# Kernel optimization log

Measured on AMD Instinct MI355X. Metric: run time of the kernel, lower is better.

Reference implementation:

```python
import jax, jax.numpy as jnp
import numpy as np

N, C, OUT, S, NS = 8192, 256, 256, 8, 16  # points, in_planes, out_planes, share_planes, nsample
MID = OUT  # mid_planes = out_planes // 1
H = OUT // S  # linear_w bottleneck width
EPS = 1e-5


def _bn(x, g, b, m, v):
    # inference-mode BatchNorm1d over last (channel) dim
    return (x - m) * jax.lax.rsqrt(v + EPS) * g + b


def _knn_idx(p, k):
    # squared euclidean distances, (N,N); indices of k nearest (self included)
    sq = jnp.sum(p * p, axis=1)
    d = sq[:, None] + sq[None, :] - 2.0 * (p @ p.T)
    return jax.lax.top_k(-jax.lax.stop_gradient(d), k)[1]  # (N, k) int32


def setup_inputs() -> dict:
    key = jax.random.key(0)
    ks = jax.random.split(key, 24)
    g = lambda i, shape, s=0.05: jax.random.normal(ks[i], shape, jnp.float32) * s
    u = lambda i, shape: jax.random.uniform(ks[i], shape, dtype=jnp.float32)
    return {
        'p': u(0, (N, 3)),
        'x': g(1, (N, C), 1.0),
        'w_q': g(2, (C, MID)), 'b_q': jnp.zeros((MID,), jnp.float32),
        'w_k': g(3, (C, MID)), 'b_k': jnp.zeros((MID,), jnp.float32),
        'w_v': g(4, (C, OUT)), 'b_v': jnp.zeros((OUT,), jnp.float32),
        'p_w1': g(5, (3, 3), 0.5), 'p_b1': jnp.zeros((3,), jnp.float32),
        'p_bn_g': u(6, (3,)) + 0.5, 'p_bn_b': g(7, (3,), 0.1),
        'p_bn_m': g(8, (3,), 0.1), 'p_bn_v': u(9, (3,)) + 0.5,
        'p_w2': g(10, (3, OUT), 0.5), 'p_b2': jnp.zeros((OUT,), jnp.float32),
        'w_bn1_g': u(11, (MID,)) + 0.5, 'w_bn1_b': g(12, (MID,), 0.1),
        'w_bn1_m': g(13, (MID,), 0.1), 'w_bn1_v': u(14, (MID,)) + 0.5,
        'w_l1_w': g(15, (MID, H)), 'w_l1_b': jnp.zeros((H,), jnp.float32),
        'w_bn2_g': u(16, (H,)) + 0.5, 'w_bn2_b': g(17, (H,), 0.1),
        'w_bn2_m': g(18, (H,), 0.1), 'w_bn2_v': u(19, (H,)) + 0.5,
        'w_l2_w': g(20, (H, H)), 'w_l2_b': jnp.zeros((H,), jnp.float32),
    }


def reference(p, x, w_q, b_q, w_k, b_k, w_v, b_v,
              p_w1, p_b1, p_bn_g, p_bn_b, p_bn_m, p_bn_v, p_w2, p_b2,
              w_bn1_g, w_bn1_b, w_bn1_m, w_bn1_v, w_l1_w, w_l1_b,
              w_bn2_g, w_bn2_b, w_bn2_m, w_bn2_v, w_l2_w, w_l2_b):
    # PointTransformerLayer forward (single point cloud, o = [N])
    xq = x @ w_q + b_q            # (N, MID)
    xk = x @ w_k + b_k            # (N, MID)
    xv = x @ w_v + b_v            # (N, OUT)

    idx = _knn_idx(p, NS)         # (N, NS) KNN neighbor indices
    pr_xyz = p[idx] - p[:, None, :]   # (N, NS, 3) relative coords (with_xyz=True)
    xk_g = xk[idx]                # (N, NS, MID) gathered keys
    xv_g = xv[idx]                # (N, NS, OUT) gathered values

    # linear_p: Linear(3,3) -> BN -> ReLU -> Linear(3, OUT)
    pr = jax.nn.relu(_bn(pr_xyz @ p_w1 + p_b1, p_bn_g, p_bn_b, p_bn_m, p_bn_v))
    pr = pr @ p_w2 + p_b2         # (N, NS, OUT)

    # einops reduce 'n ns (i j)->n ns j' with j=MID is identity since MID==OUT
    r_qk = xk_g - xq[:, None, :] + pr   # (N, NS, MID)

    # linear_w: BN -> ReLU -> Linear(MID,H) -> BN -> ReLU -> Linear(H,H)
    w = jax.nn.relu(_bn(r_qk, w_bn1_g, w_bn1_b, w_bn1_m, w_bn1_v)) @ w_l1_w + w_l1_b
    w = jax.nn.relu(_bn(w, w_bn2_g, w_bn2_b, w_bn2_m, w_bn2_v)) @ w_l2_w + w_l2_b
    w = jax.nn.softmax(w, axis=1)       # softmax over neighbors (dim=1)

    v = (xv_g + pr).reshape(N, NS, S, H)      # 'n ns (s i) -> n ns s i'
    out = jnp.einsum('ntsi,nti->nsi', v, w)   # weighted aggregation over neighbors
    return out.reshape(N, OUT)
```

## Files before the change

### kernel.cpp

```cpp
#include <hip/hip_runtime.h>
#include <hip/hip_bf16.h>
#include <math.h>

#define N_PTS 8192
#define C_IN  256
#define OUT_C 256
#define NSAMP 16
#define H_W   32
#define EPSBN 1e-5f
#define GDIM  8
#define NCELL (GDIM * GDIM * GDIM)
#define CAPC  768
#define CAP_H 40

typedef short bf16x8 __attribute__((ext_vector_type(8)));
typedef float f32x4  __attribute__((ext_vector_type(4)));

__device__ __forceinline__ float dist2(const float4 a, const float4 b) {
  float dot = a.x * b.x + a.y * b.y + a.z * b.z;
  return a.w + b.w - 2.0f * dot;
}

__device__ __forceinline__ unsigned long long make_key(float d, int j) {
  unsigned int di = __float_as_uint(d);
  unsigned int ord = ((int)di >= 0) ? (di ^ 0x80000000u) : ~di;
  return ((unsigned long long)ord << 32) | (unsigned int)j;
}

__device__ __forceinline__ void chain_insert(unsigned long long (&ak)[16], unsigned long long key) {
  if (key < ak[0]) {
    #pragma unroll
    for (int s = 0; s < 15; ++s) {
      unsigned long long mn = ak[s] < key ? ak[s] : key;
      unsigned long long nx = ak[s + 1];
      ak[s] = nx > mn ? nx : mn;
    }
    ak[15] = ak[15] < key ? ak[15] : key;
  }
}

__device__ __forceinline__ void merge16f(float (&A)[16], int m) {
  float B[16], t[16];
  #pragma unroll
  for (int s = 0; s < 16; ++s) B[s] = __shfl_xor(A[s], m, 64);
  #pragma unroll
  for (int s = 0; s < 16; ++s) t[s] = fminf(A[s], B[15 - s]);
  #pragma unroll
  for (int k = 8; k >= 1; k >>= 1) {
    #pragma unroll
    for (int s = 0; s < 16; ++s) {
      if (!(s & k)) {
        float lo = fminf(t[s], t[s | k]);
        float hi = fmaxf(t[s], t[s | k]);
        t[s] = lo; t[s | k] = hi;
      }
    }
  }
  #pragma unroll
  for (int s = 0; s < 16; ++s) A[s] = t[s];
}

__global__ __launch_bounds__(256) void prep_kernel(
    const float* __restrict__ p,
    const float* __restrict__ wq, const float* __restrict__ wk, const float* __restrict__ wv,
    const float* __restrict__ bq, const float* __restrict__ bk, const float* __restrict__ bv,
    const float* __restrict__ l1w, const float* __restrict__ l2w,
    float4* __restrict__ p4, __hip_bfloat16* __restrict__ Bp, float* __restrict__ biasp,
    __hip_bfloat16* __restrict__ l1wp, __hip_bfloat16* __restrict__ l2wp,
    int* __restrict__ hist, int* __restrict__ pt_cell) {
  int tid = blockIdx.x * blockDim.x + threadIdx.x;
  if (tid < 48 * 32 * 16 * 8) {
    int kj = tid & 7, n = (tid >> 3) & 15, kb = (tid >> 7) & 31, nt = tid >> 12;
    int k = kb * 8 + kj, col = nt * 16 + n;
    float v;
    if (col < 256)      v = wq[k * 256 + col];
    else if (col < 512) v = wk[k * 256 + (col - 256)];
    else                v = wv[k * 256 + (col - 512)];
    Bp[tid] = __float2bfloat16(v);
  }
  if (tid < 768) {
    biasp[tid] = tid < 256 ? bq[tid] : (tid < 512 ? bk[tid - 256] : bv[tid - 512]);
  }
  if (tid < 8192) {
    int kj = tid & 7, n = (tid >> 3) & 15, kb = (tid >> 7) & 31, nt = (tid >> 12) & 1;
    int k = kb * 8 + kj, col = nt * 16 + n;
    l1wp[tid] = __float2bfloat16(l1w[k * 32 + col]);
  }
  if (tid < 1024) {
    int kj = tid & 7, n = (tid >> 3) & 15, kb = (tid >> 7) & 3, nt = (tid >> 9) & 1;
    int k = kb * 8 + kj, col = nt * 16 + n;
    l2wp[tid] = __float2bfloat16(l2w[k * 32 + col]);
  }
  if (tid < N_PTS) {
    float px = p[tid * 3 + 0], py = p[tid * 3 + 1], pz = p[tid * 3 + 2];
    float sq = px * px;
    sq += py * py;
    sq += pz * pz;
    p4[tid] = make_float4(px, py, pz, sq);
    int cx = min(GDIM - 1, max(0, (int)(px * GDIM)));
    int cy = min(GDIM - 1, max(0, (int)(py * GDIM)));
    int cz = min(GDIM - 1, max(0, (int)(pz * GDIM)));
    int cell = (cz * GDIM + cy) * GDIM + cx;
    pt_cell[tid] = cell;
    atomicAdd(&hist[cell], 1);
  }
}

__global__ __launch_bounds__(512) void scan512(const int* __restrict__ hist, int* __restrict__ cell_start) {
  __shared__ int buf[NCELL];
  int t = threadIdx.x;
  buf[t] = hist[t];
  __syncthreads();
  for (int off = 1; off < NCELL; off <<= 1) {
    int add = (t >= off) ? buf[t - off] : 0;
    __syncthreads();
    buf[t] += add;
    __syncthreads();
  }
  cell_start[t + 1] = buf[t];
  if (t == 0) cell_start[0] = 0;
}

__global__ __launch_bounds__(256) void scatter_kernel(
    const float4* __restrict__ p4, const int* __restrict__ pt_cell,
    const int* __restrict__ cell_start, int* __restrict__ cursor,
    float4* __restrict__ sp4, int* __restrict__ sidx, int* __restrict__ rank) {
  int tid = blockIdx.x * blockDim.x + threadIdx.x;
  if (tid < N_PTS) {
    int c = pt_cell[tid];
    int pos = cell_start[c] + atomicAdd(&cursor[c], 1);
    sp4[pos] = p4[tid];
    sidx[pos] = tid;
    rank[tid] = pos;
  }
}

__global__ __launch_bounds__(256) void xbf_kernel(
    const float* __restrict__ x, const int* __restrict__ sidx,
    __hip_bfloat16* __restrict__ x_bf) {
  const int b = blockIdx.x;
  const int c = threadIdx.x;
  x_bf[(size_t)b * C_IN + c] = __float2bfloat16(x[(size_t)sidx[b] * C_IN + c]);
}

__global__ __launch_bounds__(256) void knn_grid(
    const float4* __restrict__ sp4, const int* __restrict__ sidx,
    const int* __restrict__ cell_start, int* __restrict__ nbr) {
  __shared__ float4 cpos[CAPC];
  __shared__ int    cidx[CAPC];
  __shared__ unsigned long long hk_s[8][CAP_H];
  __shared__ unsigned long long okey_s[8][16];
  __shared__ int cnt_s[8];
  __shared__ int cell_s0_s[27];
  __shared__ int len_s[27];
  __shared__ int pref_s[28];
  __shared__ int nc_s, total_s;

  const int cell = blockIdx.x >> 1;
  const int sub  = blockIdx.x & 1;
  const int tid = threadIdx.x;
  const int hcx = cell & 7, hcy = (cell >> 3) & 7, hcz = cell >> 6;
  const int cs = cell_start[cell], ce = cell_start[cell + 1];

  const int ax0 = max(hcx - 1, 0), ax1 = min(hcx + 1, GDIM - 1);
  const int ay0 = max(hcy - 1, 0), ay1 = min(hcy + 1, GDIM - 1);
  const int az0 = max(hcz - 1, 0), az1 = min(hcz + 1, GDIM - 1);
  const int nx = ax1 - ax0 + 1, ny = ay1 - ay0 + 1, nz = az1 - az0 + 1;
  const int nbc = nx * ny * nz;

  if (tid < nbc) {
    int cx = ax0 + tid % nx;
    int cy = ay0 + (tid / nx) % ny;
    int cz = az0 + tid / (nx * ny);
    int cc = (cz * GDIM + cy) * GDIM + cx;
    int s0 = cell_start[cc];
    cell_s0_s[tid] = s0;
    len_s[tid] = cell_start[cc + 1] - s0;
  }
  __syncthreads();
  if (tid == 0) {
    int off = 0;
    for (int m = 0; m < nbc; ++m) { pref_s[m] = off; off += len_s[m]; }
    pref_s[nbc] = off;
    nc_s = nbc;
    total_s = off;
  }
  __syncthreads();
  const int nc = nc_s, total = total_s;

  for (int idx = tid; idx < total && idx < CAPC; idx += 256) {
    int c = 0;
    while (c + 1 < nc && pref_s[c + 1] <= idx) ++c;
    int g = cell_s0_s[c] + (idx - pref_s[c]);
    cpos[idx] = sp4[g];
    cidx[idx] = sidx[g];
  }
  __syncthreads();

  const int ptl = tid >> 5, slice = tid & 31;

  for (int p0 = cs + 8 * sub; p0 < ce; p0 += 16) {
    const int np = min(8, ce - p0);
    const bool pok = ptl < np;
    const int ld = pok ? (p0 + ptl) : cs;
    const float4 pi = sp4[ld];
    const int orig = sidx[ld];

    if (tid < 8) cnt_s[tid] = 0;
    if (tid < 128) okey_s[tid >> 4][tid & 15] = ~0ULL;
    __syncthreads();

    float a[16];
    #pragma unroll
    for (int s = 0; s < 16; ++s) a[s] = 3.0e38f;
    for (int idx = slice; idx < total; idx += 32) {
      float4 q;
      if (idx < CAPC) q = cpos[idx];
      else {
        int c = 0;
        while (c + 1 < nc && pref_s[c + 1] <= idx) ++c;
        q = sp4[cell_s0_s[c] + (idx - pref_s[c])];
      }
      float d = dist2(pi, q);
      if (d < a[0]) {
        #pragma unroll
        for (int s = 0; s < 15; ++s) a[s] = fmaxf(a[s + 1], fminf(a[s], d));
        a[15] = fminf(a[15], d);
      }
    }
    float asc[16];
    #pragma unroll
    for (int s = 0; s < 16; ++s) asc[s] = a[15 - s];
    merge16f(asc, 1);
    merge16f(asc, 2);
    merge16f(asc, 4);
    merge16f(asc, 8);
    merge16f(asc, 16);
    const float d16 = asc[15];

    if (pok) {
      for (int idx = slice; idx < total; idx += 32) {
        float4 q;
        int qi;
        if (idx < CAPC) { q = cpos[idx]; qi = cidx[idx]; }
        else {
          int c = 0;
          while (c + 1 < nc && pref_s[c + 1] <= idx) ++c;
          int g = cell_s0_s[c] + (idx - pref_s[c]);
          q = sp4[g]; qi = sidx[g];
        }
        float d = dist2(pi, q);
        if (d <= d16) {
          int pos = atomicAdd(&cnt_s[ptl], 1);
          if (pos < CAP_H) hk_s[ptl][pos] = make_key(d, qi);
        }
      }
    }
    __syncthreads();

    const int cntr = cnt_s[ptl];
    const bool overflow = cntr > CAP_H;
    const int cnt = overflow ? 0 : cntr;

    if (pok) {
      for (int i = slice; i < cnt; i += 32) {
        unsigned long long key = hk_s[ptl][i];
        int rk = 0;
        for (int j = 0; j < cnt; ++j) rk += (hk_s[ptl][j] < key) ? 1 : 0;
        if (rk < 16) okey_s[ptl][rk] = key;
      }
    }
    __syncthreads();

    if (slice == 0 && pok) {
      unsigned long long akm[16];
      if (!overflow) {
        #pragma unroll
        for (int s = 0; s < 16; ++s) akm[s] = okey_s[ptl][15 - s];
      } else {
        #pragma unroll
        for (int s = 0; s < 16; ++s) akm[s] = ~0ULL;
        for (int idx = 0; idx < total; ++idx) {
          float4 q; int qi;
          if (idx < CAPC) { q = cpos[idx]; qi = cidx[idx]; }
          else {
            int c = 0;
            while (c + 1 < nc && pref_s[c + 1] <= idx) ++c;
            int g = cell_s0_s[c] + (idx - pref_s[c]);
            q = sp4[g]; qi = sidx[g];
          }
          chain_insert(akm, make_key(dist2(pi, q), qi));
        }
      }
      float r;
      if (akm[0] == ~0ULL) {
        r = 1e9f;
      } else {
        unsigned int ord = (unsigned int)(akm[0] >> 32);
        unsigned int di = (ord & 0x80000000u) ? (ord ^ 0x80000000u) : ~ord;
        float dd = __uint_as_float(di);
        r = sqrtf(fmaxf(dd, 0.f)) * 1.001f + 1e-4f;
      }
      int lx = (int)fminf(fmaxf(floorf((pi.x - r) * GDIM), 0.f), (float)(GDIM - 1));
      int ux = (int)fminf(fmaxf(floorf((pi.x + r) * GDIM), 0.f), (float)(GDIM - 1));
      int ly = (int)fminf(fmaxf(floorf((pi.y - r) * GDIM), 0.f), (float)(GDIM - 1));
      int uy = (int)fminf(fmaxf(floorf((pi.y + r) * GDIM), 0.f), (float)(GDIM - 1));
      int lz = (int)fminf(fmaxf(floorf((pi.z - r) * GDIM), 0.f), (float)(GDIM - 1));
      int uz = (int)fminf(fmaxf(floorf((pi.z + r) * GDIM), 0.f), (float)(GDIM - 1));
      if (lx < ax0 || ux > ax1 || ly < ay0 || uy > ay1 || lz < az0 || uz > az1) {
        for (int cz = lz; cz <= uz; ++cz)
          for (int cy = ly; cy <= uy; ++cy)
            for (int cx = lx; cx <= ux; ++cx) {
              if (cx >= ax0 && cx <= ax1 && cy >= ay0 && cy <= ay1 && cz >= az0 && cz <= az1)
                continue;
              int cc = (cz * GDIM + cy) * GDIM + cx;
              int s0 = cell_start[cc], e0 = cell_start[cc + 1];
              for (int k = s0; k < e0; ++k) {
                float4 q = sp4[k];
                chain_insert(akm, make_key(dist2(pi, q), sidx[k]));
              }
            }
      }
      #pragma unroll
      for (int s = 0; s < 16; ++s) nbr[orig * NSAMP + s] = (int)(akm[s] & 0xFFFFFFFFu);
    }
    __syncthreads();
  }
}

__global__ __launch_bounds__(256) void gemm_qkv_mfma(
    const __hip_bfloat16* __restrict__ x_bf, const __hip_bfloat16* __restrict__ Bp,
    const float* __restrict__ biasp, __hip_bfloat16* __restrict__ xqkv) {
  const int w = threadIdx.x >> 6;
  const int lane = threadIdx.x & 63;
  const int gw = blockIdx.x * 4 + w;
  const int m0 = (gw & 127) * 64;
  const int nt4 = (gw >> 7) * 4;
  const int n = lane & 15, q = lane >> 4;

  f32x4 acc[4][4];
  #pragma unroll
  for (int mi = 0; mi < 4; ++mi)
    #pragma unroll
    for (int ni = 0; ni < 4; ++ni) acc[mi][ni] = (f32x4){0.f, 0.f, 0.f, 0.f};

  for (int k0 = 0; k0 < 256; k0 += 32) {
    bf16x8 af[4], bfr[4];
    #pragma unroll
    for (int mi = 0; mi < 4; ++mi)
      af[mi] = *(const bf16x8*)&x_bf[(size_t)(m0 + mi * 16 + n) * 256 + k0 + q * 8];
    #pragma unroll
    for (int ni = 0; ni < 4; ++ni)
      bfr[ni] = *(const bf16x8*)&Bp[(size_t)(nt4 + ni) * 4096 + (k0 >> 3) * 128 + q * 128 + n * 8];
    #pragma unroll
    for (int mi = 0; mi < 4; ++mi)
      #pragma unroll
      for (int ni = 0; ni < 4; ++ni)
        acc[mi][ni] = __builtin_amdgcn_mfma_f32_16x16x32_bf16(af[mi], bfr[ni], acc[mi][ni], 0, 0, 0);
  }
  #pragma unroll
  for (int ni = 0; ni < 4; ++ni) {
    int col = (nt4 + ni) * 16 + n;
    float b = biasp[col];
    #pragma unroll
    for (int mi = 0; mi < 4; ++mi)
      #pragma unroll
      for (int r = 0; r < 4; ++r)
        xqkv[(size_t)(m0 + mi * 16 + q * 4 + r) * 768 + col] = __float2bfloat16(acc[mi][ni][r] + b);
  }
}

__global__ __launch_bounds__(256) void fused_pt(
    const float4* __restrict__ sp4, const int* __restrict__ sidx, const int* __restrict__ rank,
    const __hip_bfloat16* __restrict__ xqkv, const int* __restrict__ nbr,
    const float* __restrict__ pw1, const float* __restrict__ pb1,
    const float* __restrict__ pbng, const float* __restrict__ pbnb,
    const float* __restrict__ pbnm, const float* __restrict__ pbnv,
    const float* __restrict__ pw2, const float* __restrict__ pb2,
    const float* __restrict__ bn1g, const float* __restrict__ bn1b,
    const float* __restrict__ bn1m, const float* __restrict__ bn1v,
    const __hip_bfloat16* __restrict__ l1wp, const float* __restrict__ l1b,
    const float* __restrict__ bn2g, const float* __restrict__ bn2b,
    const float* __restrict__ bn2m, const float* __restrict__ bn2v,
    const __hip_bfloat16* __restrict__ l2wp, const float* __restrict__ l2b,
    float* __restrict__ out) {
  __shared__ __align__(16) __hip_bfloat16 a_s[NSAMP][264];
  __shared__ __align__(16) __hip_bfloat16 h1_s[NSAMP][40];
  __shared__ float w_s[NSAMP][33];
  __shared__ float q3_s[NSAMP][4];
  __shared__ int jn[NSAMP];

  const int b = blockIdx.x;
  const int i = sidx[b];
  const int tid = threadIdx.x;

  if (tid < NSAMP) {
    int j = nbr[i * NSAMP + tid];
    int k = rank[j];
    jn[tid] = k;
    float4 pj = sp4[k];
    float4 pc = sp4[b];
    float rx = pj.x - pc.x;
    float ry = pj.y - pc.y;
    float rz = pj.z - pc.z;
    #pragma unroll
    for (int c3 = 0; c3 < 3; ++c3) {
      float t = rx * pw1[0 * 3 + c3] + ry * pw1[1 * 3 + c3] + rz * pw1[2 * 3 + c3] + pb1[c3];
      t = (t - pbnm[c3]) * rsqrtf(pbnv[c3] + EPSBN) * pbng[c3] + pbnb[c3];
      q3_s[tid][c3] = fmaxf(t, 0.f);
    }
  }
  __syncthreads();

  const int c = tid;
  const float xq_c = __bfloat162float(xqkv[(size_t)b * 768 + c]);
  const float s1 = bn1g[c] * rsqrtf(bn1v[c] + EPSBN);
  const float o1 = bn1b[c] - bn1m[c] * s1;
  const float w2c0 = pw2[c], w2c1 = pw2[256 + c], w2c2 = pw2[512 + c];
  const float pb2c = pb2[c];
  #pragma unroll
  for (int t = 0; t < NSAMP; ++t) {
    int k = jn[t];
    float prv = q3_s[t][0] * w2c0 + q3_s[t][1] * w2c1 + q3_s[t][2] * w2c2 + pb2c;
    float xkv = __bfloat162float(xqkv[(size_t)k * 768 + 256 + c]);
    float r = xkv - xq_c + prv;
    a_s[t][c] = __float2bfloat16(fmaxf(r * s1 + o1, 0.f));
  }
  __syncthreads();

  const int wv_ = tid >> 6;
  const int lane = tid & 63;
  const int nn = lane & 15, q = lane >> 4;
  if (wv_ < 2) {
    f32x4 acc = {0.f, 0.f, 0.f, 0.f};
    #pragma unroll
    for (int k0 = 0; k0 < 256; k0 += 32) {
      bf16x8 a = *(const bf16x8*)&a_s[nn][k0 + q * 8];
      bf16x8 bb = *(const bf16x8*)&l1wp[wv_ * 4096 + (k0 >> 3) * 128 + q * 128 + nn * 8];
      acc = __builtin_amdgcn_mfma_f32_16x16x32_bf16(a, bb, acc, 0, 0, 0);
    }
    int h = wv_ * 16 + nn;
    float s2 = bn2g[h] * rsqrtf(bn2v[h] + EPSBN);
    float o2 = bn2b[h] - bn2m[h] * s2;
    float l1bh = l1b[h];
    #pragma unroll
    for (int r = 0; r < 4; ++r)
      h1_s[q * 4 + r][h] = __float2bfloat16(fmaxf((acc[r] + l1bh) * s2 + o2, 0.f));
  }
  __syncthreads();

  if (wv_ < 2) {
    bf16x8 a = *(const bf16x8*)&h1_s[nn][q * 8];
    bf16x8 bb = *(const bf16x8*)&l2wp[wv_ * 512 + q * 128 + nn * 8];
    f32x4 z = {0.f, 0.f, 0.f, 0.f};
    f32x4 d = __builtin_amdgcn_mfma_f32_16x16x32_bf16(a, bb, z, 0, 0, 0);
    int h = wv_ * 16 + nn;
    float l2bh = l2b[h];
    #pragma unroll
    for (int r = 0; r < 4; ++r) w_s[q * 4 + r][h] = d[r] + l2bh;
  }
  __syncthreads();

  if (tid < H_W) {
    int h = tid;
    float m = -1e30f;
    #pragma unroll
    for (int t = 0; t < NSAMP; ++t) m = fmaxf(m, w_s[t][h]);
    float e[NSAMP];
    float ssum = 0.f;
    #pragma unroll
    for (int t = 0; t < NSAMP; ++t) { e[t] = __expf(w_s[t][h] - m); ssum += e[t]; }
    float inv = 1.f / ssum;
    #pragma unroll
    for (int t = 0; t < NSAMP; ++t) w_s[t][h] = e[t] * inv;
  }
  __syncthreads();

  const int h = c & 31;
  float acc6 = 0.f;
  #pragma unroll
  for (int t = 0; t < NSAMP; ++t) {
    int k = jn[t];
    float xv = __bfloat162float(xqkv[(size_t)k * 768 + 512 + c]);
    float prv = q3_s[t][0] * w2c0 + q3_s[t][1] * w2c1 + q3_s[t][2] * w2c2 + pb2c;
    acc6 += (xv + prv) * w_s[t][h];
  }
  out[(size_t)i * OUT_C + c] = acc6;
}

extern "C" void kernel_launch(void* const* d_in, const int* in_sizes, int n_in,
                              void* d_out, int out_size, void* d_ws, size_t ws_size,
                              hipStream_t stream) {
  const float* p    = (const float*)d_in[0];
  const float* x    = (const float*)d_in[1];
  const float* wq   = (const float*)d_in[2];
  const float* bq   = (const float*)d_in[3];
  const float* wk   = (const float*)d_in[4];
  const float* bk   = (const float*)d_in[5];
  const float* wv   = (const float*)d_in[6];
  const float* bv   = (const float*)d_in[7];
  const float* pw1  = (const float*)d_in[8];
  const float* pb1  = (const float*)d_in[9];
  const float* pbng = (const float*)d_in[10];
  const float* pbnb = (const float*)d_in[11];
  const float* pbnm = (const float*)d_in[12];
  const float* pbnv = (const float*)d_in[13];
  const float* pw2  = (const float*)d_in[14];
  const float* pb2  = (const float*)d_in[15];
  const float* bn1g = (const float*)d_in[16];
  const float* bn1b = (const float*)d_in[17];
  const float* bn1m = (const float*)d_in[18];
  const float* bn1v = (const float*)d_in[19];
  const float* l1w  = (const float*)d_in[20];
  const float* l1b  = (const float*)d_in[21];
  const float* bn2g = (const float*)d_in[22];
  const float* bn2b = (const float*)d_in[23];
  const float* bn2m = (const float*)d_in[24];
  const float* bn2v = (const float*)d_in[25];
  const float* l2w  = (const float*)d_in[26];
  const float* l2b  = (const float*)d_in[27];
  float* out = (float*)d_out;

  char* ws = (char*)d_ws;
  float4* p4       = (float4*)(ws + 0x000000);
  float*  biasp    = (float*)(ws + 0x040000);
  int*    hist     = (int*)(ws + 0x042000);
  int*    cursor   = (int*)(ws + 0x042800);
  int*    cell_st  = (int*)(ws + 0x043000);
  int*    pt_cell  = (int*)(ws + 0x044000);
  float4* sp4      = (float4*)(ws + 0x050000);
  int*    sidx     = (int*)(ws + 0x070000);
  __hip_bfloat16* l1wp = (__hip_bfloat16*)(ws + 0x080000);
  __hip_bfloat16* l2wp = (__hip_bfloat16*)(ws + 0x084000);
  int*    rank     = (int*)(ws + 0x088000);
  int*    nbr      = (int*)(ws + 0x090000);
  __hip_bfloat16* Bp   = (__hip_bfloat16*)(ws + 0x110000);
  __hip_bfloat16* x_bf = (__hip_bfloat16*)(ws + 0x170000);
  __hip_bfloat16* xqkv = (__hip_bfloat16*)(ws + 0x570000);

  hipMemsetAsync(ws + 0x042000, 0, 0x1000, stream);
  prep_kernel<<<dim3(768), dim3(256), 0, stream>>>(
      p, wq, wk, wv, bq, bk, bv, l1w, l2w, p4, Bp, biasp, l1wp, l2wp,
      hist, pt_cell);
  scan512<<<dim3(1), dim3(NCELL), 0, stream>>>(hist, cell_st);
  scatter_kernel<<<dim3(32), dim3(256), 0, stream>>>(p4, pt_cell, cell_st, cursor, sp4, sidx, rank);
  xbf_kernel<<<dim3(N_PTS), dim3(256), 0, stream>>>(x, sidx, x_bf);
  gemm_qkv_mfma<<<dim3(384), dim3(256), 0, stream>>>(x_bf, Bp, biasp, xqkv);
  knn_grid<<<dim3(NCELL * 2), dim3(256), 0, stream>>>(sp4, sidx, cell_st, nbr);
  fused_pt<<<dim3(N_PTS), dim3(256), 0, stream>>>(
      sp4, sidx, rank, xqkv, nbr, pw1, pb1, pbng, pbnb, pbnm, pbnv, pw2, pb2,
      bn1g, bn1b, bn1m, bn1v, l1wp, l1b, bn2g, bn2b, bn2m, bn2v, l2wp, l2b, out);
}
```

Before: 213.7 us.

## Merge scan/scatter, fuse QKV GEMM with KNN launch, vectorize fused_pt channels

The grid scan and the point scatter now run in one kernel. Each of 16 blocks recomputes the prefix sum and only block 0 writes cell_start. The separate bf16 conversion kernel is removed: the QKV GEMM gathers fp32 x rows by sorted index and converts them in registers, and it shares one launch with the KNN blocks so the two independent stages can overlap. In fused_pt each thread now handles 8 channels for half of the neighbours with 16-byte bf16 loads, and the per-channel partial sums are combined through a shared-memory tree reduction. This cuts launches and intermediate traffic but adds redundant scan work, extra barriers and shared memory use.

```diff
diff --git a/kernel.cpp b/kernel.cpp
--- a/kernel.cpp
+++ b/kernel.cpp
@@ -12,6 +12,8 @@
 #define NCELL (GDIM * GDIM * GDIM)
 #define CAPC  768
 #define CAP_H 40
+#define GEMM_BLOCKS 384
+#define KNN_BLOCKS (NCELL * 2)
 
 typedef short bf16x8 __attribute__((ext_vector_type(8)));
 typedef float f32x4  __attribute__((ext_vector_type(4)));
@@ -58,6 +60,16 @@
   }
   #pragma unroll
   for (int s = 0; s < 16; ++s) A[s] = t[s];
+}
+
+__device__ __forceinline__ float b2f(short s) {
+  return __uint_as_float(((unsigned int)(unsigned short)s) << 16);
+}
+__device__ __forceinline__ short f2b(float v) {
+  __hip_bfloat16 h = __float2bfloat16(v);
+  short s;
+  __builtin_memcpy(&s, &h, 2);
+  return s;
 }
 
 __global__ __launch_bounds__(256) void prep_kernel(
@@ -106,9 +118,12 @@
   }
 }
 
-__global__ __launch_bounds__(512) void scan512(const int* __restrict__ hist, int* __restrict__ cell_start) {
+__global__ __launch_bounds__(512) void scatter_scan(
+    const float4* __restrict__ p4, const int* __restrict__ pt_cell,
+    const int* __restrict__ hist, int* __restrict__ cell_start, int* __restrict__ cursor,
+    float4* __restrict__ sp4, int* __restrict__ sidx, int* __restrict__ rank) {
   __shared__ int buf[NCELL];
-  int t = threadIdx.x;
+  const int t = threadIdx.x;
   buf[t] = hist[t];
   __syncthreads();
   for (int off = 1; off < NCELL; off <<= 1) {
@@ -117,35 +132,24 @@
     buf[t] += add;
     __syncthreads();
   }
-  cell_start[t + 1] = buf[t];
-  if (t == 0) cell_start[0] = 0;
-}
-
-__global__ __launch_bounds__(256) void scatter_kernel(
-    const float4* __restrict__ p4, const int* __restrict__ pt_cell,
-    const int* __restrict__ cell_start, int* __restrict__ cursor,
-    float4* __restrict__ sp4, int* __restrict__ sidx, int* __restrict__ rank) {
-  int tid = blockIdx.x * blockDim.x + threadIdx.x;
-  if (tid < N_PTS) {
-    int c = pt_cell[tid];
-    int pos = cell_start[c] + atomicAdd(&cursor[c], 1);
-    sp4[pos] = p4[tid];
-    sidx[pos] = tid;
-    rank[tid] = pos;
-  }
-}
-
-__global__ __launch_bounds__(256) void xbf_kernel(
-    const float* __restrict__ x, const int* __restrict__ sidx,
-    __hip_bfloat16* __restrict__ x_bf) {
-  const int b = blockIdx.x;
-  const int c = threadIdx.x;
-  x_bf[(size_t)b * C_IN + c] = __float2bfloat16(x[(size_t)sidx[b] * C_IN + c]);
-}
-
-__global__ __launch_bounds__(256) void knn_grid(
+  if (blockIdx.x == 0) {
+    cell_start[t + 1] = buf[t];
+    if (t == 0) cell_start[0] = 0;
+  }
+  const int pid = blockIdx.x * 512 + t;
+  const int c = pt_cell[pid];
+  const int start = (c == 0) ? 0 : buf[c - 1];
+  const int pos = start + atomicAdd(&cursor[c], 1);
+  sp4[pos] = p4[pid];
+  sidx[pos] = pid;
+  rank[pid] = pos;
+}
+
+__global__ __launch_bounds__(256) void mid_kernel(
     const float4* __restrict__ sp4, const int* __restrict__ sidx,
-    const int* __restrict__ cell_start, int* __restrict__ nbr) {
+    const int* __restrict__ cell_start, int* __restrict__ nbr,
+    const float* __restrict__ x, const __hip_bfloat16* __restrict__ Bp,
+    const float* __restrict__ biasp, __hip_bfloat16* __restrict__ xqkv) {
   __shared__ float4 cpos[CAPC];
   __shared__ int    cidx[CAPC];
   __shared__ unsigned long long hk_s[8][CAP_H];
@@ -156,9 +160,63 @@
   __shared__ int pref_s[28];
   __shared__ int nc_s, total_s;
 
-  const int cell = blockIdx.x >> 1;
-  const int sub  = blockIdx.x & 1;
   const int tid = threadIdx.x;
+
+  if (blockIdx.x < GEMM_BLOCKS) {
+    const int w = tid >> 6;
+    const int lane = tid & 63;
+    const int gw = blockIdx.x * 4 + w;
+    const int m0 = (gw & 127) * 64;
+    const int nt4 = (gw >> 7) * 4;
+    const int n = lane & 15, q = lane >> 4;
+
+    int o[4];
+    #pragma unroll
+    for (int mi = 0; mi < 4; ++mi) o[mi] = sidx[m0 + mi * 16 + n];
+
+    f32x4 acc[4][4];
+    #pragma unroll
+    for (int mi = 0; mi < 4; ++mi)
+      #pragma unroll
+      for (int ni = 0; ni < 4; ++ni) acc[mi][ni] = (f32x4){0.f, 0.f, 0.f, 0.f};
+
+    for (int k0 = 0; k0 < 256; k0 += 32) {
+      bf16x8 af[4], bfr[4];
+      #pragma unroll
+      for (int mi = 0; mi < 4; ++mi) {
+        const float* xr = &x[(size_t)o[mi] * 256 + k0 + q * 8];
+        float4 xa = *(const float4*)xr;
+        float4 xb = *(const float4*)(xr + 4);
+        af[mi][0] = f2b(xa.x); af[mi][1] = f2b(xa.y);
+        af[mi][2] = f2b(xa.z); af[mi][3] = f2b(xa.w);
+        af[mi][4] = f2b(xb.x); af[mi][5] = f2b(xb.y);
+        af[mi][6] = f2b(xb.z); af[mi][7] = f2b(xb.w);
+      }
+      #pragma unroll
+      for (int ni = 0; ni < 4; ++ni)
+        bfr[ni] = *(const bf16x8*)&Bp[(size_t)(nt4 + ni) * 4096 + (k0 >> 3) * 128 + q * 128 + n * 8];
+      #pragma unroll
+      for (int mi = 0; mi < 4; ++mi)
+        #pragma unroll
+        for (int ni = 0; ni < 4; ++ni)
+          acc[mi][ni] = __builtin_amdgcn_mfma_f32_16x16x32_bf16(af[mi], bfr[ni], acc[mi][ni], 0, 0, 0);
+    }
+    #pragma unroll
+    for (int ni = 0; ni < 4; ++ni) {
+      int col = (nt4 + ni) * 16 + n;
+      float b = biasp[col];
+      #pragma unroll
+      for (int mi = 0; mi < 4; ++mi)
+        #pragma unroll
+        for (int r = 0; r < 4; ++r)
+          xqkv[(size_t)(m0 + mi * 16 + q * 4 + r) * 768 + col] = __float2bfloat16(acc[mi][ni][r] + b);
+    }
+    return;
+  }
+
+  const int kb = blockIdx.x - GEMM_BLOCKS;
+  const int cell = kb >> 1;
+  const int sub  = kb & 1;
   const int hcx = cell & 7, hcy = (cell >> 3) & 7, hcz = cell >> 6;
   const int cs = cell_start[cell], ce = cell_start[cell + 1];
 
@@ -328,48 +386,6 @@
   }
 }
 
-__global__ __launch_bounds__(256) void gemm_qkv_mfma(
-    const __hip_bfloat16* __restrict__ x_bf, const __hip_bfloat16* __restrict__ Bp,
-    const float* __restrict__ biasp, __hip_bfloat16* __restrict__ xqkv) {
-  const int w = threadIdx.x >> 6;
-  const int lane = threadIdx.x & 63;
-  const int gw = blockIdx.x * 4 + w;
-  const int m0 = (gw & 127) * 64;
-  const int nt4 = (gw >> 7) * 4;
-  const int n = lane & 15, q = lane >> 4;
-
-  f32x4 acc[4][4];
-  #pragma unroll
-  for (int mi = 0; mi < 4; ++mi)
-    #pragma unroll
-    for (int ni = 0; ni < 4; ++ni) acc[mi][ni] = (f32x4){0.f, 0.f, 0.f, 0.f};
-
-  for (int k0 = 0; k0 < 256; k0 += 32) {
-    bf16x8 af[4], bfr[4];
-    #pragma unroll
-    for (int mi = 0; mi < 4; ++mi)
-      af[mi] = *(const bf16x8*)&x_bf[(size_t)(m0 + mi * 16 + n) * 256 + k0 + q * 8];
-    #pragma unroll
-    for (int ni = 0; ni < 4; ++ni)
-      bfr[ni] = *(const bf16x8*)&Bp[(size_t)(nt4 + ni) * 4096 + (k0 >> 3) * 128 + q * 128 + n * 8];
-    #pragma unroll
-    for (int mi = 0; mi < 4; ++mi)
-      #pragma unroll
-      for (int ni = 0; ni < 4; ++ni)
-        acc[mi][ni] = __builtin_amdgcn_mfma_f32_16x16x32_bf16(af[mi], bfr[ni], acc[mi][ni], 0, 0, 0);
-  }
-  #pragma unroll
-  for (int ni = 0; ni < 4; ++ni) {
-    int col = (nt4 + ni) * 16 + n;
-    float b = biasp[col];
-    #pragma unroll
-    for (int mi = 0; mi < 4; ++mi)
-      #pragma unroll
-      for (int r = 0; r < 4; ++r)
-        xqkv[(size_t)(m0 + mi * 16 + q * 4 + r) * 768 + col] = __float2bfloat16(acc[mi][ni][r] + b);
-  }
-}
-
 __global__ __launch_bounds__(256) void fused_pt(
     const float4* __restrict__ sp4, const int* __restrict__ sidx, const int* __restrict__ rank,
     const __hip_bfloat16* __restrict__ xqkv, const int* __restrict__ nbr,
@@ -389,6 +405,7 @@
   __shared__ float w_s[NSAMP][33];
   __shared__ float q3_s[NSAMP][4];
   __shared__ int jn[NSAMP];
+  __shared__ float psum[8][264];
 
   const int b = blockIdx.x;
   const int i = sidx[b];
@@ -412,19 +429,39 @@
   }
   __syncthreads();
 
-  const int c = tid;
-  const float xq_c = __bfloat162float(xqkv[(size_t)b * 768 + c]);
-  const float s1 = bn1g[c] * rsqrtf(bn1v[c] + EPSBN);
-  const float o1 = bn1b[c] - bn1m[c] * s1;
-  const float w2c0 = pw2[c], w2c1 = pw2[256 + c], w2c2 = pw2[512 + c];
-  const float pb2c = pb2[c];
-  #pragma unroll
-  for (int t = 0; t < NSAMP; ++t) {
+  const int cg = (tid & 31) * 8;
+  const int grp = tid >> 5;
+  float xqv[8], s1v[8], o1v[8], w20v[8], w21v[8], w22v[8], pb2v[8];
+  {
+    bf16x8 xq8 = *(const bf16x8*)&xqkv[(size_t)b * 768 + cg];
+    #pragma unroll
+    for (int u = 0; u < 8; ++u) {
+      int c = cg + u;
+      xqv[u] = b2f(xq8[u]);
+      float s1 = bn1g[c] * rsqrtf(bn1v[c] + EPSBN);
+      s1v[u] = s1;
+      o1v[u] = bn1b[c] - bn1m[c] * s1;
+      w20v[u] = pw2[c];
+      w21v[u] = pw2[256 + c];
+      w22v[u] = pw2[512 + c];
+      pb2v[u] = pb2[c];
+    }
+  }
+
+  #pragma unroll
+  for (int pass = 0; pass < 2; ++pass) {
+    int t = grp + pass * 8;
     int k = jn[t];
-    float prv = q3_s[t][0] * w2c0 + q3_s[t][1] * w2c1 + q3_s[t][2] * w2c2 + pb2c;
-    float xkv = __bfloat162float(xqkv[(size_t)k * 768 + 256 + c]);
-    float r = xkv - xq_c + prv;
-    a_s[t][c] = __float2bfloat16(fmaxf(r * s1 + o1, 0.f));
+    float q30 = q3_s[t][0], q31 = q3_s[t][1], q32 = q3_s[t][2];
+    bf16x8 xk8 = *(const bf16x8*)&xqkv[(size_t)k * 768 + 256 + cg];
+    bf16x8 av;
+    #pragma unroll
+    for (int u = 0; u < 8; ++u) {
+      float prv = q30 * w20v[u] + q31 * w21v[u] + q32 * w22v[u] + pb2v[u];
+      float r = b2f(xk8[u]) - xqv[u] + prv;
+      av[u] = f2b(fmaxf(r * s1v[u] + o1v[u], 0.f));
+    }
+    *(bf16x8*)&a_s[t][cg] = av;
   }
   __syncthreads();
 
@@ -476,16 +513,41 @@
   }
   __syncthreads();
 
-  const int h = c & 31;
-  float acc6 = 0.f;
-  #pragma unroll
-  for (int t = 0; t < NSAMP; ++t) {
+  const int hb = cg & 31;
+  float acc8[8];
+  #pragma unroll
+  for (int u = 0; u < 8; ++u) acc8[u] = 0.f;
+  #pragma unroll
+  for (int pass = 0; pass < 2; ++pass) {
+    int t = grp + pass * 8;
     int k = jn[t];
-    float xv = __bfloat162float(xqkv[(size_t)k * 768 + 512 + c]);
-    float prv = q3_s[t][0] * w2c0 + q3_s[t][1] * w2c1 + q3_s[t][2] * w2c2 + pb2c;
-    acc6 += (xv + prv) * w_s[t][h];
-  }
-  out[(size_t)i * OUT_C + c] = acc6;
+    float q30 = q3_s[t][0], q31 = q3_s[t][1], q32 = q3_s[t][2];
+    bf16x8 xv8 = *(const bf16x8*)&xqkv[(size_t)k * 768 + 512 + cg];
+    #pragma unroll
+    for (int u = 0; u < 8; ++u) {
+      float prv = q30 * w20v[u] + q31 * w21v[u] + q32 * w22v[u] + pb2v[u];
+      acc8[u] += (b2f(xv8[u]) + prv) * w_s[t][hb + u];
+    }
+  }
+  #pragma unroll
+  for (int u = 0; u < 8; ++u) psum[grp][cg + u] = acc8[u];
+  __syncthreads();
+  if (grp < 4) {
+    #pragma unroll
+    for (int u = 0; u < 8; ++u) psum[grp][cg + u] += psum[grp + 4][cg + u];
+  }
+  __syncthreads();
+  if (grp < 2) {
+    #pragma unroll
+    for (int u = 0; u < 8; ++u) psum[grp][cg + u] += psum[grp + 2][cg + u];
+  }
+  __syncthreads();
+  if (grp < 1) {
+    #pragma unroll
+    for (int u = 0; u < 8; ++u) psum[0][cg + u] += psum[1][cg + u];
+  }
+  __syncthreads();
+  out[(size_t)i * OUT_C + tid] = psum[0][tid];
 }
 
 extern "C" void kernel_launch(void* const* d_in, const int* in_sizes, int n_in,
@@ -535,18 +597,16 @@
   int*    rank     = (int*)(ws + 0x088000);
   int*    nbr      = (int*)(ws + 0x090000);
   __hip_bfloat16* Bp   = (__hip_bfloat16*)(ws + 0x110000);
-  __hip_bfloat16* x_bf = (__hip_bfloat16*)(ws + 0x170000);
   __hip_bfloat16* xqkv = (__hip_bfloat16*)(ws + 0x570000);
 
   hipMemsetAsync(ws + 0x042000, 0, 0x1000, stream);
   prep_kernel<<<dim3(768), dim3(256), 0, stream>>>(
       p, wq, wk, wv, bq, bk, bv, l1w, l2w, p4, Bp, biasp, l1wp, l2wp,
       hist, pt_cell);
-  scan512<<<dim3(1), dim3(NCELL), 0, stream>>>(hist, cell_st);
-  scatter_kernel<<<dim3(32), dim3(256), 0, stream>>>(p4, pt_cell, cell_st, cursor, sp4, sidx, rank);
-  xbf_kernel<<<dim3(N_PTS), dim3(256), 0, stream>>>(x, sidx, x_bf);
-  gemm_qkv_mfma<<<dim3(384), dim3(256), 0, stream>>>(x_bf, Bp, biasp, xqkv);
-  knn_grid<<<dim3(NCELL * 2), dim3(256), 0, stream>>>(sp4, sidx, cell_st, nbr);
+  scatter_scan<<<dim3(16), dim3(512), 0, stream>>>(
+      p4, pt_cell, hist, cell_st, cursor, sp4, sidx, rank);
+  mid_kernel<<<dim3(GEMM_BLOCKS + KNN_BLOCKS), dim3(256), 0, stream>>>(
+      sp4, sidx, cell_st, nbr, x, Bp, biasp, xqkv);
   fused_pt<<<dim3(N_PTS), dim3(256), 0, stream>>>(
       sp4, sidx, rank, xqkv, nbr, pw1, pb1, pbng, pbnb, pbnm, pbnv, pw2, pb2,
       bn1g, bn1b, bn1m, bn1v, l1wp, l1b, bn2g, bn2b, bn2m, bn2v, l2wp, l2b, out);
```

Result: slower. 234.0 us (+9.5%).
